# Kernel optimization log

Measured on AMD Instinct MI355X. Metric: run time of the kernel, lower is better.

The kernel has to match this reference:

```python
import jax, jax.numpy as jnp
import numpy as np

B, N, C_IN, C_OUT, K = 8, 4096, 64, 128, 15
RADIUS = 0.1            # 2.5 * grid_size(0.04) * sigma(1.0)
MAX_NN = 34
KP_EXTENT = 0.04        # point_influence = prev_grid_size * sigma
KERNEL_RADIUS = 1.5 * KP_EXTENT
NEG_SLOPE = 0.2
BN_EPS = 1e-5


def setup_inputs() -> dict:
    key = jax.random.key(0)
    k1, k2, k3, k4 = jax.random.split(key, 4)
    xyz = jax.random.uniform(k1, (B, N, 3), dtype=jnp.float32)
    feats = jax.random.normal(k2, (B, N, C_IN), dtype=jnp.float32)
    # fixed kernel point disposition inside the kernel ball (requires_grad=False in torch)
    kp = jax.random.normal(k3, (K, 3), dtype=jnp.float32)
    kp = kp / (jnp.linalg.norm(kp, axis=-1, keepdims=True) + 1e-6) * KERNEL_RADIUS * 0.7
    kp = kp.at[0].set(0.0)  # center point
    std = float(np.sqrt(2.0 / (K * C_IN)))
    weight = jax.random.normal(k4, (K, C_IN, C_OUT), dtype=jnp.float32) * std
    gamma = jnp.ones((C_OUT,), dtype=jnp.float32)
    beta = jnp.zeros((C_OUT,), dtype=jnp.float32)
    return {"xyz": xyz, "feats": feats, "K_points": kp, "weight": weight,
            "gamma": gamma, "beta": beta}


def _ball_query(xyz):
    # xyz: [B, N, 3] -> flat neighbor idx [B*N, MAX_NN] into the concatenated
    # point array; missing neighbors get shadow index B*N.
    b_, n_, _ = xyz.shape
    shadow = b_ * n_

    def per_cloud(pts, b):
        d2 = jnp.sum((pts[:, None, :] - pts[None, :, :]) ** 2, axis=-1)  # [N, N]
        neg_d2, idx = jax.lax.top_k(-d2, MAX_NN)                         # k nearest
        valid = (-neg_d2) <= RADIUS ** 2
        return jnp.where(valid, idx + b * n_, shadow)

    return jax.vmap(per_cloud)(xyz, jnp.arange(b_)).reshape(b_ * n_, MAX_NN)


def _kpconv_block(xyz, feats, K_points, weight, gamma, beta):
    b_, n_, _ = xyz.shape
    pts = xyz.reshape(b_ * n_, 3)
    f = feats.reshape(b_ * n_, C_IN)
    nidx = _ball_query(xyz)                                   # [M, nn]
    # shadow point far away / zero features (KPConv_ops)
    pts_pad = jnp.concatenate([pts, jnp.full((1, 3), 1e6, pts.dtype)], axis=0)
    f_pad = jnp.concatenate([f, jnp.zeros((1, C_IN), f.dtype)], axis=0)
    nbr = pts_pad[nidx] - pts[:, None, :]                     # [M, nn, 3] relative coords
    sq = jnp.sum((nbr[:, :, None, :] - K_points) ** 2, -1)    # [M, nn, K]
    w = jnp.maximum(1.0 - jnp.sqrt(sq) / KP_EXTENT, 0.0)      # linear influence
    nf = f_pad[nidx]                                          # [M, nn, Cin]
    wf = jnp.einsum('mnk,mnc->mkc', w, nf)                    # per-kernel-point feats
    out = jnp.einsum('mkc,kcd->md', wf, weight)               # [M, Cout]
    # FastBatchNorm1d (training-mode batch stats, biased var) + LeakyReLU
    mu = out.mean(axis=0)
    var = out.var(axis=0)
    out = (out - mu) * jax.lax.rsqrt(var + BN_EPS) * gamma + beta
    out = jnp.where(out >= 0, out, NEG_SLOPE * out)
    return out.reshape(b_, n_, C_OUT)


def reference(xyz, feats, K_points, weight, gamma, beta):
    return _kpconv_block(xyz, feats, K_points, weight, gamma, beta)
```

## Files before the change

### kernel.cpp

```cpp
#include <hip/hip_runtime.h>


#define NB     8
#define NPTS   4096
#define M_TOT  32768
#define CIN    64
#define COUT   128
#define NKP    15
#define MAXNN  34
#define NNPAD  36
#define NCELL  1728
#define R2EFF  (0.082f * 0.082f)
#define KP_INV 25.0f
#define NEG_SLOPE 0.2f
#define KTOT   960
#define WFPAD  968

typedef float f32x4_t __attribute__((ext_vector_type(4)));
typedef short bf16x8_t __attribute__((ext_vector_type(8)));

__device__ __forceinline__ unsigned short f2bf(float f) {
  union { float f; unsigned u; } v; v.f = f;
  unsigned r = v.u + 0x7FFF + ((v.u >> 16) & 1);
  return (unsigned short)(r >> 16);
}
__device__ __forceinline__ float bf2f(unsigned short s) {
  union { unsigned u; float f; } v; v.u = ((unsigned)s) << 16; return v.f;
}
__device__ __forceinline__ int cell_of(float x, float y, float z) {
  int cx = (int)(x * 12.f); cx = cx > 11 ? 11 : cx;
  int cy = (int)(y * 12.f); cy = cy > 11 ? 11 : cy;
  int cz = (int)(z * 12.f); cz = cz > 11 ? 11 : cz;
  return (cz * 12 + cy) * 12 + cx;
}

__global__ __launch_bounds__(256) void k0a_hist(
    const float* __restrict__ xyz, int* __restrict__ cellcnt)
{
  const int pt = blockIdx.x * 256 + threadIdx.x;
  const float x = xyz[pt * 3], y = xyz[pt * 3 + 1], z = xyz[pt * 3 + 2];
  const int b = pt >> 12;
  atomicAdd(&cellcnt[b * NCELL + cell_of(x, y, z)], 1);
}

__global__ __launch_bounds__(256) void k0b_scan_kW(
    const int* __restrict__ cellcnt, int* __restrict__ cellstart,
    const float* __restrict__ W, unsigned short* __restrict__ Wt)
{
  if (blockIdx.x >= 8) {
    const int idx = (blockIdx.x - 8) * 256 + threadIdx.x;
    const int n = idx & 127, kg = idx >> 7;
    union { unsigned short s[8]; uint4 v; } u;
    #pragma unroll
    for (int j = 0; j < 8; j++)
      u.s[j] = f2bf(W[(size_t)(kg * 8 + j) * COUT + n]);
    *(uint4*)&Wt[(size_t)n * KTOT + kg * 8] = u.v;
    return;
  }
  __shared__ int ps[256];
  const int b = blockIdx.x, t = threadIdx.x;
  int local[7], s = 0;
  #pragma unroll
  for (int i = 0; i < 7; i++) {
    const int cid = t * 7 + i;
    const int c = (cid < NCELL) ? cellcnt[b * NCELL + cid] : 0;
    local[i] = c; s += c;
  }
  ps[t] = s; __syncthreads();
  for (int off = 1; off < 256; off <<= 1) {
    int v = (t >= off) ? ps[t - off] : 0;
    __syncthreads();
    ps[t] += v;
    __syncthreads();
  }
  int run = ps[t] - s;
  #pragma unroll
  for (int i = 0; i < 7; i++) {
    const int cid = t * 7 + i;
    if (cid < NCELL) { cellstart[b * 1729 + cid] = run; run += local[i]; }
  }
  if (t == 255) cellstart[b * 1729 + NCELL] = ps[255];
}

__global__ __launch_bounds__(256) void k0c_scatter(
    const float* __restrict__ xyz, const float* __restrict__ feats,
    const int* __restrict__ cellstart, int* __restrict__ cellfill,
    int* __restrict__ qorder, float4* __restrict__ xyzs,
    unsigned short* __restrict__ fsorted)
{
  const int pt = blockIdx.x * 256 + threadIdx.x;
  const float x = xyz[pt * 3], y = xyz[pt * 3 + 1], z = xyz[pt * 3 + 2];
  const int b = pt >> 12;
  const int cid = cell_of(x, y, z);
  const int slot = atomicAdd(&cellfill[b * NCELL + cid], 1);
  const int pos = b * NPTS + cellstart[b * 1729 + cid] + slot;
  qorder[pos] = pt;
  xyzs[pos] = make_float4(x, y, z, 0.f);
  const float* src = &feats[(size_t)pt * CIN];
  uint4* dst = (uint4*)&fsorted[(size_t)pos * CIN];
  #pragma unroll
  for (int g = 0; g < 8; g++) {
    float4 a = *(const float4*)(src + g * 8);
    float4 c = *(const float4*)(src + g * 8 + 4);
    union { unsigned short s[8]; uint4 v; } u;
    u.s[0] = f2bf(a.x); u.s[1] = f2bf(a.y); u.s[2] = f2bf(a.z); u.s[3] = f2bf(a.w);
    u.s[4] = f2bf(c.x); u.s[5] = f2bf(c.y); u.s[6] = f2bf(c.z); u.s[7] = f2bf(c.w);
    dst[g] = u.v;
  }
}

__global__ __launch_bounds__(256) void k1_grid(
    const float4* __restrict__ xyzs, const int* __restrict__ cellstart,
    unsigned short* __restrict__ nlist, int* __restrict__ ncnt)
{
  const int m = blockIdx.x * 4 + (threadIdx.x >> 6);
  const int L = threadIdx.x & 63;
  const int b = m >> 12;
  const float4 Q = xyzs[m];
  int cx = (int)(Q.x * 12.f); cx = cx > 11 ? 11 : cx;
  int cy = (int)(Q.y * 12.f); cy = cy > 11 ? 11 : cy;
  int cz = (int)(Q.z * 12.f); cz = cz > 11 ? 11 : cz;

  int r0v = 0, lenv = 0;
  if (L < 9) {
    const int ny = cy + (L % 3) - 1;
    const int nz = cz + (L / 3) - 1;
    if (ny >= 0 && ny < 12 && nz >= 0 && nz < 12) {
      const int xlo = cx > 0 ? cx - 1 : 0;
      const int xhi = cx < 11 ? cx + 1 : 11;
      const int base = b * 1729 + (nz * 12 + ny) * 12;
      r0v  = cellstart[base + xlo];
      lenv = cellstart[base + xhi + 1] - r0v;
    }
  }
  int r0a[9], pfxa[10];
  pfxa[0] = 0;
  #pragma unroll
  for (int i = 0; i < 9; i++) {
    r0a[i] = __shfl(r0v, i);
    pfxa[i + 1] = pfxa[i] + __shfl(lenv, i);
  }
  const int T = pfxa[9];

  int cnt = 0;
  for (int tb = 0; tb < T; tb += 64) {
    const int t = tb + L;
    bool hit = false; int pos = 0;
    if (t < T) {
      int r = 0;
      #pragma unroll
      for (int i = 1; i < 9; i++) r += (t >= pfxa[i]);
      pos = r0a[r] + t - pfxa[r];
      const float4 P = xyzs[b * NPTS + pos];
      const float dx = P.x - Q.x, dy = P.y - Q.y, dz = P.z - Q.z;
      hit = (dx * dx + dy * dy + dz * dz) <= R2EFF;
    }
    const unsigned long long mask = __ballot(hit);
    if (hit) {
      const int slot = cnt + __popcll(mask & ((1ull << L) - 1ull));
      if (slot < MAXNN)
        nlist[(size_t)m * MAXNN + slot] = (unsigned short)(b * NPTS + pos);
    }
    cnt += __popcll(mask);
  }
  if (L == 0) ncnt[m] = cnt > MAXNN ? MAXNN : cnt;
}

__global__ __launch_bounds__(256, 2) void k2_conv(
    const float4* __restrict__ xyzs, const unsigned short* __restrict__ fsorted,
    const float* __restrict__ kpts, const unsigned short* __restrict__ nlist,
    const int* __restrict__ ncnt, const int* __restrict__ qorder,
    const unsigned short* __restrict__ Wt, float* __restrict__ out,
    float* __restrict__ psum, float* __restrict__ psumsq)
{
  __shared__ float  w2[16][NNPAD][16];
  __shared__ short  wf[16][WFPAD];
  __shared__ int    gidx[16][NNPAD];
  __shared__ float4 qd[16];
  __shared__ int    qm[16];
  __shared__ int    cnts[16], cnt4[16];
  __shared__ float  kp[NKP][4];

  const int tid = threadIdx.x;
  const int w   = tid >> 6;
  const int L   = tid & 63;
  const int m0  = blockIdx.x * 16;

  if (tid < NKP * 3) {
    int k = tid / 3, c = tid - k * 3;
    kp[k][c] = kpts[tid];
  }
  if (tid < 16) {
    qd[tid] = xyzs[m0 + tid];
    qm[tid] = qorder[m0 + tid];
    const int c = ncnt[m0 + tid];
    cnts[tid] = c;
    cnt4[tid] = (c + 3) & ~3;
  }
  __syncthreads();

  #pragma unroll
  for (int rep = 0; rep < 3; rep++) {
    const int p = rep * 256 + tid;
    if (p < 16 * NNPAD) {
      const int q  = p / NNPAD;
      const int nn = p - q * NNPAD;
      float wv[16];
      int g;
      if (nn < cnts[q]) {
        g = (int)nlist[(size_t)(m0 + q) * MAXNN + nn];
        const float4 P = xyzs[g];
        const float4 Qx = qd[q];
        const float rx = P.x - Qx.x, ry = P.y - Qx.y, rz = P.z - Qx.z;
        #pragma unroll
        for (int k = 0; k < NKP; k++) {
          const float dx = rx - kp[k][0];
          const float dy = ry - kp[k][1];
          const float dz = rz - kp[k][2];
          wv[k] = fmaxf(1.f - sqrtf(dx*dx + dy*dy + dz*dz) * KP_INV, 0.f);
        }
        wv[15] = 0.f;
      } else {
        g = m0 + q;
        #pragma unroll
        for (int k = 0; k < 16; k++) wv[k] = 0.f;
      }
      gidx[q][nn] = g;
      float* dst = w2[q][nn];
      *(float4*)(dst + 0)  = *(float4*)(wv + 0);
      *(float4*)(dst + 4)  = *(float4*)(wv + 4);
      *(float4*)(dst + 8)  = *(float4*)(wv + 8);
      *(float4*)(dst + 12) = *(float4*)(wv + 12);
    }
  }
  __syncthreads();

  for (int qi = 0; qi < 4; qi++) {
    const int q = w * 4 + qi;
    const int c4 = cnt4[q];
    float acc[NKP];
    #pragma unroll
    for (int k = 0; k < NKP; k++) acc[k] = 0.f;

    for (int nn = 0; nn < c4; nn += 4) {
      const int4 gg = *(const int4*)&gidx[q][nn];
      const float f0 = bf2f(fsorted[(size_t)gg.x * CIN + L]);
      const float f1 = bf2f(fsorted[(size_t)gg.y * CIN + L]);
      const float f2 = bf2f(fsorted[(size_t)gg.z * CIN + L]);
      const float f3 = bf2f(fsorted[(size_t)gg.w * CIN + L]);
      const float* r0 = w2[q][nn + 0];
      const float* r1 = w2[q][nn + 1];
      const float* r2 = w2[q][nn + 2];
      const float* r3 = w2[q][nn + 3];
      #pragma unroll
      for (int k = 0; k < NKP; k++)
        acc[k] += r0[k] * f0 + r1[k] * f1 + r2[k] * f2 + r3[k] * f3;
    }
    #pragma unroll
    for (int k = 0; k < NKP; k++)
      wf[q][k * 64 + L] = (short)f2bf(acc[k]);
  }
  __syncthreads();

  const int ln = L & 15;
  const int kh = L >> 4;
  const int colbase = w * 32;

  f32x4_t acc2[2];
  acc2[0] = (f32x4_t){0.f, 0.f, 0.f, 0.f};
  acc2[1] = (f32x4_t){0.f, 0.f, 0.f, 0.f};

  const unsigned short* Bp0 = &Wt[(size_t)(colbase + ln) * KTOT + kh * 8];
  const unsigned short* Bp1 = Bp0 + 16 * KTOT;
  const short* Ap = &wf[ln][kh * 8];

  #pragma unroll 3
  for (int kk = 0; kk < 30; kk++) {
    const int ko = kk * 32;
    bf16x8_t b0 = *(const bf16x8_t*)(Bp0 + ko);
    bf16x8_t b1 = *(const bf16x8_t*)(Bp1 + ko);
    bf16x8_t a0 = *(const bf16x8_t*)(Ap + ko);
    acc2[0] = __builtin_amdgcn_mfma_f32_16x16x32_bf16(a0, b0, acc2[0], 0, 0, 0);
    acc2[1] = __builtin_amdgcn_mfma_f32_16x16x32_bf16(a0, b1, acc2[1], 0, 0, 0);
  }

  float s0 = 0.f, q0 = 0.f, s1 = 0.f, q1 = 0.f;
  #pragma unroll
  for (int j = 0; j < 4; j++) {
    s0 += acc2[0][j]; q0 += acc2[0][j] * acc2[0][j];
    s1 += acc2[1][j]; q1 += acc2[1][j] * acc2[1][j];
  }
  s0 += __shfl_xor(s0, 16); s0 += __shfl_xor(s0, 32);
  q0 += __shfl_xor(q0, 16); q0 += __shfl_xor(q0, 32);
  s1 += __shfl_xor(s1, 16); s1 += __shfl_xor(s1, 32);
  q1 += __shfl_xor(q1, 16); q1 += __shfl_xor(q1, 32);
  if (kh == 0) {
    atomicAdd(&psum[colbase + ln], s0);
    atomicAdd(&psumsq[colbase + ln], q0);
    atomicAdd(&psum[colbase + 16 + ln], s1);
    atomicAdd(&psumsq[colbase + 16 + ln], q1);
  }

  #pragma unroll
  for (int c = 0; c < 2; c++) {
    #pragma unroll
    for (int j = 0; j < 4; j++) {
      const int row = kh * 4 + j;
      out[(size_t)qm[row] * COUT + colbase + c * 16 + ln] = acc2[c][j];
    }
  }
}

__global__ __launch_bounds__(256) void k4_norm(
    float* __restrict__ out, const float* __restrict__ psum,
    const float* __restrict__ psumsq, const float* __restrict__ gamma,
    const float* __restrict__ beta)
{
  __shared__ float a_s[128], b_s[128];
  if (threadIdx.x < 128) {
    const int d = threadIdx.x;
    double mu  = (double)psum[d] / (double)M_TOT;
    double var = (double)psumsq[d] / (double)M_TOT - mu * mu;
    float rstd = (float)(1.0 / sqrt(var + 1e-5));
    float a = rstd * gamma[d];
    a_s[d] = a;
    b_s[d] = beta[d] - (float)mu * a;
  }
  __syncthreads();
  const int idx = blockIdx.x * 256 + threadIdx.x;
  float4 v = ((const float4*)out)[idx];
  const int d0 = (idx * 4) & 127;
  float y0 = v.x * a_s[d0 + 0] + b_s[d0 + 0];
  float y1 = v.y * a_s[d0 + 1] + b_s[d0 + 1];
  float y2 = v.z * a_s[d0 + 2] + b_s[d0 + 2];
  float y3 = v.w * a_s[d0 + 3] + b_s[d0 + 3];
  v.x = y0 >= 0.f ? y0 : NEG_SLOPE * y0;
  v.y = y1 >= 0.f ? y1 : NEG_SLOPE * y1;
  v.z = y2 >= 0.f ? y2 : NEG_SLOPE * y2;
  v.w = y3 >= 0.f ? y3 : NEG_SLOPE * y3;
  ((float4*)out)[idx] = v;
}

extern "C" void kernel_launch(void* const* d_in, const int* in_sizes, int n_in,
                              void* d_out, int out_size, void* d_ws,
                              size_t ws_size, hipStream_t stream)
{
  const float* xyz   = (const float*)d_in[0];
  const float* feats = (const float*)d_in[1];
  const float* kpts  = (const float*)d_in[2];
  const float* W     = (const float*)d_in[3];
  const float* gamma = (const float*)d_in[4];
  const float* beta  = (const float*)d_in[5];
  float* out = (float*)d_out;

  char* ws = (char*)d_ws;
  int*            cellcnt   = (int*)(ws + 0);
  int*            cellfill  = (int*)(ws + 55296);
  float*          psum      = (float*)(ws + 110592);
  float*          psumsq    = (float*)(ws + 111104);
  int*            cellstart = (int*)(ws + 111616);
  int*            qorder    = (int*)(ws + 167040);
  float4*         xyzs      = (float4*)(ws + 298112);
  unsigned short* fsorted   = (unsigned short*)(ws + 822400);
  unsigned short* Wt        = (unsigned short*)(ws + 5016704);
  unsigned short* nlist     = (unsigned short*)(ws + 5262464);
  int*            ncnt      = (int*)(ws + 7490688);

  hipMemsetAsync(ws, 0, 111616, stream);

  k0a_hist   <<< 128, 256, 0, stream>>>(xyz, cellcnt);
  k0b_scan_kW<<<  68, 256, 0, stream>>>(cellcnt, cellstart, W, Wt);
  k0c_scatter<<< 128, 256, 0, stream>>>(xyz, feats, cellstart, cellfill,
                                        qorder, xyzs, fsorted);
  k1_grid    <<<8192, 256, 0, stream>>>(xyzs, cellstart, nlist, ncnt);
  k2_conv    <<<2048, 256, 0, stream>>>(xyzs, fsorted, kpts, nlist, ncnt,
                                        qorder, Wt, out, psum, psumsq);
  k4_norm    <<<(out_size / 4) / 256, 256, 0, stream>>>(out, psum, psumsq,
                                                        gamma, beta);
}
```

Baseline: 209.8 us.

## Compute per-kernel-point feature aggregation with MFMA and cap neighbors at 32

Replaces the scalar FMA loop that aggregates neighbor features per kernel point with a bf16 MFMA: influence weights and gathered features are staged transposed in shared memory and multiplied as 16x32 by 32x64 tiles. To fit the 32-wide MFMA K dimension, the neighbor cap drops from 34 to 32, and the weight matrix is re-laid out as channel-major with 16 kernel-point slots (K padded to 1024). This changes results whenever a point has more than 32 neighbors within the radius, and influence weights are now rounded to bf16.

```diff
diff --git a/kernel.cpp b/kernel.cpp
--- a/kernel.cpp
+++ b/kernel.cpp
@@ -7,14 +7,14 @@
 #define CIN    64
 #define COUT   128
 #define NKP    15
-#define MAXNN  34
-#define NNPAD  36
+#define NN32   32
 #define NCELL  1728
 #define R2EFF  (0.082f * 0.082f)
 #define KP_INV 25.0f
 #define NEG_SLOPE 0.2f
-#define KTOT   960
-#define WFPAD  968
+#define KCP    1024
+#define WFPAD  1032
+#define NP     40
 
 typedef float f32x4_t __attribute__((ext_vector_type(4)));
 typedef short bf16x8_t __attribute__((ext_vector_type(8)));
@@ -23,9 +23,6 @@
   union { float f; unsigned u; } v; v.f = f;
   unsigned r = v.u + 0x7FFF + ((v.u >> 16) & 1);
   return (unsigned short)(r >> 16);
-}
-__device__ __forceinline__ float bf2f(unsigned short s) {
-  union { unsigned u; float f; } v; v.u = ((unsigned)s) << 16; return v.f;
 }
 __device__ __forceinline__ int cell_of(float x, float y, float z) {
   int cx = (int)(x * 12.f); cx = cx > 11 ? 11 : cx;
@@ -49,12 +46,14 @@
 {
   if (blockIdx.x >= 8) {
     const int idx = (blockIdx.x - 8) * 256 + threadIdx.x;
-    const int n = idx & 127, kg = idx >> 7;
-    union { unsigned short s[8]; uint4 v; } u;
-    #pragma unroll
-    for (int j = 0; j < 8; j++)
-      u.s[j] = f2bf(W[(size_t)(kg * 8 + j) * COUT + n]);
-    *(uint4*)&Wt[(size_t)n * KTOT + kg * 8] = u.v;
+    const int d = idx & 127, c = idx >> 7;
+    union { unsigned short s[16]; uint4 v[2]; } u;
+    #pragma unroll
+    for (int k = 0; k < NKP; k++)
+      u.s[k] = f2bf(W[(size_t)k * (CIN * COUT) + c * COUT + d]);
+    u.s[15] = 0;
+    uint4* dst = (uint4*)&Wt[(size_t)d * KCP + c * 16];
+    dst[0] = u.v[0]; dst[1] = u.v[1];
     return;
   }
   __shared__ int ps[256];
@@ -158,12 +157,12 @@
     const unsigned long long mask = __ballot(hit);
     if (hit) {
       const int slot = cnt + __popcll(mask & ((1ull << L) - 1ull));
-      if (slot < MAXNN)
-        nlist[(size_t)m * MAXNN + slot] = (unsigned short)(b * NPTS + pos);
+      if (slot < NN32)
+        nlist[(size_t)m * NN32 + slot] = (unsigned short)(b * NPTS + pos);
     }
     cnt += __popcll(mask);
   }
-  if (L == 0) ncnt[m] = cnt > MAXNN ? MAXNN : cnt;
+  if (L == 0) ncnt[m] = cnt > NN32 ? NN32 : cnt;
 }
 
 __global__ __launch_bounds__(256, 2) void k2_conv(
@@ -173,12 +172,13 @@
     const unsigned short* __restrict__ Wt, float* __restrict__ out,
     float* __restrict__ psum, float* __restrict__ psumsq)
 {
-  __shared__ float  w2[16][NNPAD][16];
   __shared__ short  wf[16][WFPAD];
-  __shared__ int    gidx[16][NNPAD];
+  __shared__ short  wA[16][16][NP];
+  __shared__ short  FT[4][64][NP];
+  __shared__ int    gidx[16][NN32];
   __shared__ float4 qd[16];
   __shared__ int    qm[16];
-  __shared__ int    cnts[16], cnt4[16];
+  __shared__ int    cnts[16];
   __shared__ float  kp[NKP][4];
 
   const int tid = threadIdx.x;
@@ -193,89 +193,86 @@
   if (tid < 16) {
     qd[tid] = xyzs[m0 + tid];
     qm[tid] = qorder[m0 + tid];
-    const int c = ncnt[m0 + tid];
-    cnts[tid] = c;
-    cnt4[tid] = (c + 3) & ~3;
+    cnts[tid] = ncnt[m0 + tid];
   }
   __syncthreads();
 
   #pragma unroll
-  for (int rep = 0; rep < 3; rep++) {
+  for (int rep = 0; rep < 2; rep++) {
     const int p = rep * 256 + tid;
-    if (p < 16 * NNPAD) {
-      const int q  = p / NNPAD;
-      const int nn = p - q * NNPAD;
-      float wv[16];
-      int g;
-      if (nn < cnts[q]) {
-        g = (int)nlist[(size_t)(m0 + q) * MAXNN + nn];
-        const float4 P = xyzs[g];
-        const float4 Qx = qd[q];
-        const float rx = P.x - Qx.x, ry = P.y - Qx.y, rz = P.z - Qx.z;
-        #pragma unroll
-        for (int k = 0; k < NKP; k++) {
-          const float dx = rx - kp[k][0];
-          const float dy = ry - kp[k][1];
-          const float dz = rz - kp[k][2];
-          wv[k] = fmaxf(1.f - sqrtf(dx*dx + dy*dy + dz*dz) * KP_INV, 0.f);
-        }
-        wv[15] = 0.f;
-      } else {
-        g = m0 + q;
-        #pragma unroll
-        for (int k = 0; k < 16; k++) wv[k] = 0.f;
+    const int q  = p >> 5;
+    const int nn = p & 31;
+    if (nn < cnts[q]) {
+      const int g = (int)nlist[(size_t)(m0 + q) * NN32 + nn];
+      gidx[q][nn] = g;
+      const float4 P = xyzs[g];
+      const float4 Qx = qd[q];
+      const float rx = P.x - Qx.x, ry = P.y - Qx.y, rz = P.z - Qx.z;
+      #pragma unroll
+      for (int k = 0; k < NKP; k++) {
+        const float dx = rx - kp[k][0];
+        const float dy = ry - kp[k][1];
+        const float dz = rz - kp[k][2];
+        const float wv =
+            fmaxf(1.f - sqrtf(dx * dx + dy * dy + dz * dz) * KP_INV, 0.f);
+        wA[q][k][nn] = (short)f2bf(wv);
       }
-      gidx[q][nn] = g;
-      float* dst = w2[q][nn];
-      *(float4*)(dst + 0)  = *(float4*)(wv + 0);
-      *(float4*)(dst + 4)  = *(float4*)(wv + 4);
-      *(float4*)(dst + 8)  = *(float4*)(wv + 8);
-      *(float4*)(dst + 12) = *(float4*)(wv + 12);
+      wA[q][15][nn] = 0;
+    } else {
+      gidx[q][nn] = m0 + q;
+      #pragma unroll
+      for (int k = 0; k < 16; k++) wA[q][k][nn] = 0;
     }
   }
   __syncthreads();
+
+  const int ln = L & 15;
+  const int kh = L >> 4;
 
   for (int qi = 0; qi < 4; qi++) {
     const int q = w * 4 + qi;
-    const int c4 = cnt4[q];
-    float acc[NKP];
-    #pragma unroll
-    for (int k = 0; k < NKP; k++) acc[k] = 0.f;
-
-    for (int nn = 0; nn < c4; nn += 4) {
-      const int4 gg = *(const int4*)&gidx[q][nn];
-      const float f0 = bf2f(fsorted[(size_t)gg.x * CIN + L]);
-      const float f1 = bf2f(fsorted[(size_t)gg.y * CIN + L]);
-      const float f2 = bf2f(fsorted[(size_t)gg.z * CIN + L]);
-      const float f3 = bf2f(fsorted[(size_t)gg.w * CIN + L]);
-      const float* r0 = w2[q][nn + 0];
-      const float* r1 = w2[q][nn + 1];
-      const float* r2 = w2[q][nn + 2];
-      const float* r3 = w2[q][nn + 3];
+    #pragma unroll
+    for (int i = 0; i < 8; i++) {
+      const int4 gg = *(const int4*)&gidx[q][i * 4];
+      const unsigned short f0 = fsorted[(size_t)gg.x * CIN + L];
+      const unsigned short f1 = fsorted[(size_t)gg.y * CIN + L];
+      const unsigned short f2 = fsorted[(size_t)gg.z * CIN + L];
+      const unsigned short f3 = fsorted[(size_t)gg.w * CIN + L];
+      union { unsigned short s[4]; unsigned long long d; } u;
+      u.s[0] = f0; u.s[1] = f1; u.s[2] = f2; u.s[3] = f3;
+      *(unsigned long long*)&FT[w][L][i * 4] = u.d;
+    }
+    bf16x8_t a = *(const bf16x8_t*)&wA[q][ln][kh * 8];
+    f32x4_t aq[4];
+    #pragma unroll
+    for (int t = 0; t < 4; t++) aq[t] = (f32x4_t){0.f, 0.f, 0.f, 0.f};
+    #pragma unroll
+    for (int t = 0; t < 4; t++) {
+      bf16x8_t bb = *(const bf16x8_t*)&FT[w][t * 16 + ln][kh * 8];
+      aq[t] = __builtin_amdgcn_mfma_f32_16x16x32_bf16(a, bb, aq[t], 0, 0, 0);
+    }
+    #pragma unroll
+    for (int t = 0; t < 4; t++) {
+      union { unsigned short s[4]; unsigned long long d; } u;
       #pragma unroll
-      for (int k = 0; k < NKP; k++)
-        acc[k] += r0[k] * f0 + r1[k] * f1 + r2[k] * f2 + r3[k] * f3;
-    }
-    #pragma unroll
-    for (int k = 0; k < NKP; k++)
-      wf[q][k * 64 + L] = (short)f2bf(acc[k]);
+      for (int j = 0; j < 4; j++) u.s[j] = f2bf(aq[t][j]);
+      *(unsigned long long*)&wf[q][(t * 16 + ln) * 16 + kh * 4] = u.d;
+    }
   }
   __syncthreads();
 
-  const int ln = L & 15;
-  const int kh = L >> 4;
   const int colbase = w * 32;
 
   f32x4_t acc2[2];
   acc2[0] = (f32x4_t){0.f, 0.f, 0.f, 0.f};
   acc2[1] = (f32x4_t){0.f, 0.f, 0.f, 0.f};
 
-  const unsigned short* Bp0 = &Wt[(size_t)(colbase + ln) * KTOT + kh * 8];
-  const unsigned short* Bp1 = Bp0 + 16 * KTOT;
+  const unsigned short* Bp0 = &Wt[(size_t)(colbase + ln) * KCP + kh * 8];
+  const unsigned short* Bp1 = Bp0 + 16 * KCP;
   const short* Ap = &wf[ln][kh * 8];
 
-  #pragma unroll 3
-  for (int kk = 0; kk < 30; kk++) {
+  #pragma unroll 4
+  for (int kk = 0; kk < 32; kk++) {
     const int ko = kk * 32;
     bf16x8_t b0 = *(const bf16x8_t*)(Bp0 + ko);
     bf16x8_t b1 = *(const bf16x8_t*)(Bp1 + ko);
@@ -363,13 +360,13 @@
   float4*         xyzs      = (float4*)(ws + 298112);
   unsigned short* fsorted   = (unsigned short*)(ws + 822400);
   unsigned short* Wt        = (unsigned short*)(ws + 5016704);
-  unsigned short* nlist     = (unsigned short*)(ws + 5262464);
-  int*            ncnt      = (int*)(ws + 7490688);
+  unsigned short* nlist     = (unsigned short*)(ws + 5278848);
+  int*            ncnt      = (int*)(ws + 7376000);
 
   hipMemsetAsync(ws, 0, 111616, stream);
 
   k0a_hist   <<< 128, 256, 0, stream>>>(xyz, cellcnt);
-  k0b_scan_kW<<<  68, 256, 0, stream>>>(cellcnt, cellstart, W, Wt);
+  k0b_scan_kW<<<  40, 256, 0, stream>>>(cellcnt, cellstart, W, Wt);
   k0c_scatter<<< 128, 256, 0, stream>>>(xyz, feats, cellstart, cellfill,
                                         qorder, xyzs, fsorted);
   k1_grid    <<<8192, 256, 0, stream>>>(xyzs, cellstart, nlist, ncnt);
```

New measurement: 202.8 us. 3.3% less time.
